# Optimization experiments

Measured on AMD Instinct MI355X. Metric: run time of the kernel, lower is better.

The kernel has to match this reference:

```python
import jax, jax.numpy as jnp
import numpy as np

N_NODES = 100000
N_EDGES = 1200000
D = 64
BN_EPS = 1e-5


def setup_inputs() -> dict:
    key = jax.random.key(0)
    ks = jax.random.split(key, 6)
    x = jax.random.normal(ks[0], (N_NODES, D), dtype=jnp.float32)
    edge_index = jax.random.randint(ks[1], (2, N_EDGES), 0, N_NODES, dtype=jnp.int64)
    # Linear params (Kaiming-uniform style scale)
    lim = 1.0 / np.sqrt(D)
    W = jax.random.uniform(ks[2], (D, D), dtype=jnp.float32, minval=-lim, maxval=lim)
    b = jax.random.uniform(ks[3], (D,), dtype=jnp.float32, minval=-lim, maxval=lim)
    gamma = jnp.ones((D,), dtype=jnp.float32)
    beta = jnp.zeros((D,), dtype=jnp.float32)
    C = jax.random.normal(ks[4], (D, D), dtype=jnp.float32) * 0.1
    return {"x": x, "edge_index": edge_index, "W": W, "b": b,
            "gamma": gamma, "beta": beta, "C": C}


def reference(x, edge_index, W, b, gamma, beta, C):
    n = x.shape[0]
    src, dst = edge_index[0], edge_index[1]
    # SimpleConv(aggr='mean', combine_root='sum'): mean over incoming messages + root
    msg_sum = jax.ops.segment_sum(x[src], dst, num_segments=n)            # [N, D]
    deg = jax.ops.segment_sum(jnp.ones_like(src, dtype=x.dtype), dst, num_segments=n)
    agg = msg_sum / jnp.maximum(deg, 1.0)[:, None]
    h = x + agg
    # Linear
    h = h @ W.T + b
    # BatchNorm1d (training mode: batch stats, biased variance)
    mean = jnp.mean(h, axis=0)
    var = jnp.mean((h - mean) ** 2, axis=0)
    h = (h - mean) * jax.lax.rsqrt(var + BN_EPS) * gamma + beta
    # AsymSwiGLU gate
    gate = jax.nn.sigmoid(h @ C)
    return gate * h
```

## Files before the change

kernel.cpp:

```cpp
#include <hip/hip_runtime.h>
#include <math.h>

#define D 64
#define BN_EPS 1e-5f

#define NBITS 7
#define BINSZ 128
#define MAXBINS 800
#define CAP 2048
#define CHUNK 4096
#define BUCKET 48
#define OP 68
#define WP 72

typedef short bf16x8 __attribute__((ext_vector_type(8)));
typedef float f32x4 __attribute__((ext_vector_type(4)));

__device__ __forceinline__ unsigned f2bf(float f) {
    unsigned u = __float_as_uint(f);
    return (u + 0x7FFFu + ((u >> 16) & 1u)) >> 16;
}
__device__ __forceinline__ float bf2f(unsigned short h) {
    return __uint_as_float(((unsigned)h) << 16);
}
__device__ __forceinline__ bf16x8 cvt8f(const float* __restrict__ p) {
    float4 a = ((const float4*)p)[0];
    float4 b = ((const float4*)p)[1];
    bf16x8 r;
    r[0] = (short)f2bf(a.x); r[1] = (short)f2bf(a.y);
    r[2] = (short)f2bf(a.z); r[3] = (short)f2bf(a.w);
    r[4] = (short)f2bf(b.x); r[5] = (short)f2bf(b.y);
    r[6] = (short)f2bf(b.z); r[7] = (short)f2bf(b.w);
    return r;
}
__device__ __forceinline__ void cvtrow16(const float* __restrict__ src,
                                         unsigned short* dst) {
    float4 a = ((const float4*)src)[0], b = ((const float4*)src)[1];
    float4 c = ((const float4*)src)[2], d = ((const float4*)src)[3];
    uint4 o0, o1;
    o0.x = f2bf(a.x) | (f2bf(a.y) << 16);
    o0.y = f2bf(a.z) | (f2bf(a.w) << 16);
    o0.z = f2bf(b.x) | (f2bf(b.y) << 16);
    o0.w = f2bf(b.z) | (f2bf(b.w) << 16);
    o1.x = f2bf(c.x) | (f2bf(c.y) << 16);
    o1.y = f2bf(c.z) | (f2bf(c.w) << 16);
    o1.z = f2bf(d.x) | (f2bf(d.y) << 16);
    o1.w = f2bf(d.z) | (f2bf(d.w) << 16);
    ((uint4*)dst)[0] = o0;
    ((uint4*)dst)[1] = o1;
}

__global__ __launch_bounds__(256) void xhalf_kernel(
    const float* __restrict__ x, unsigned short* __restrict__ xh, long long n8) {
    long long t = (long long)blockIdx.x * 256 + threadIdx.x;
    if (t >= n8) return;
    const float4* rp = (const float4*)(x + t * 8);
    float4 a = rp[0], b = rp[1];
    uint4 o;
    o.x = f2bf(a.x) | (f2bf(a.y) << 16);
    o.y = f2bf(a.z) | (f2bf(a.w) << 16);
    o.z = f2bf(b.x) | (f2bf(b.y) << 16);
    o.w = f2bf(b.z) | (f2bf(b.w) << 16);
    *(uint4*)(xh + t * 8) = o;
}

__global__ __launch_bounds__(1024) void binA_kernel(
    const int* __restrict__ ei, int* __restrict__ binCursor,
    unsigned* __restrict__ binBuf, int E, int nbins) {
    __shared__ unsigned short pos[CHUNK];
    __shared__ int hist[MAXBINS];
    __shared__ int base[MAXBINS];
    int tid = threadIdx.x;
    int c0 = blockIdx.x * CHUNK;

    for (int i = tid; i < nbins; i += 1024) hist[i] = 0;
    __syncthreads();

#pragma unroll
    for (int k = 0; k < CHUNK / 1024; ++k) {
        int i = k * 1024 + tid;
        int e = c0 + i;
        if (e < E) {
            int dst = ei[E + e];
            pos[i] = (unsigned short)atomicAdd(&hist[dst >> NBITS], 1);
        }
    }
    __syncthreads();

    for (int b = tid; b < nbins; b += 1024) {
        int h = hist[b];
        base[b] = h > 0 ? atomicAdd(&binCursor[b * 16], h) : 0;
    }
    __syncthreads();

#pragma unroll
    for (int k = 0; k < CHUNK / 1024; ++k) {
        int i = k * 1024 + tid;
        int e = c0 + i;
        if (e < E) {
            int src = ei[e];
            int dst = ei[E + e];
            int b = dst >> NBITS;
            int idx = base[b] + (int)pos[i];
            if (idx < CAP)
                binBuf[(size_t)b * CAP + idx] =
                    ((unsigned)src << NBITS) | (unsigned)(dst & (BINSZ - 1));
        }
    }
}

__global__ __launch_bounds__(256) void binSort_kernel(
    const unsigned* __restrict__ binBuf, const int* __restrict__ binCursor,
    int* __restrict__ csr, int* __restrict__ cnt, int N) {
    __shared__ int hist[BINSZ];
    int bin = blockIdx.x, tid = threadIdx.x;
    int nodeBase = bin << NBITS;
    int nrows = N - nodeBase; if (nrows > BINSZ) nrows = BINSZ;
    if (tid < BINSZ) hist[tid] = 0;
    __syncthreads();
    int nE = binCursor[bin * 16]; if (nE > CAP) nE = CAP;
    const unsigned* eb = binBuf + (size_t)bin * CAP;
    for (int i = tid; i < nE; i += 256) {
        unsigned r = eb[i];
        int dl = (int)(r & (BINSZ - 1));
        int src = (int)(r >> NBITS);
        int p = atomicAdd(&hist[dl], 1);
        if (p < BUCKET) csr[(size_t)(nodeBase + dl) * BUCKET + p] = src;
    }
    __syncthreads();
    for (int r = tid; r < nrows; r += 256) cnt[nodeBase + r] = hist[r];
}

__global__ __launch_bounds__(256) void gather_kernel(
    const unsigned short* __restrict__ xh,
    const int* __restrict__ csr, const int* __restrict__ cnt,
    float* __restrict__ hpre, int N) {
    int node = blockIdx.x * 4 + (threadIdx.x >> 6);
    if (node >= N) return;
    int l = threadIdx.x & 63;
    int c = l & 15;
    int g = l >> 4;
    int deg = cnt[node];
    deg = __builtin_amdgcn_readfirstlane(deg);
    int trips = deg < BUCKET ? deg : BUCKET;
    int sidx = l < BUCKET ? csr[(size_t)node * BUCKET + l] : 0;
    float a0 = 0.f, a1 = 0.f, a2 = 0.f, a3 = 0.f;
    if (trips > 0) {
        int nq = (trips + 3) >> 2;
        int last = trips - 1;
        uint2 v[12];
#pragma unroll
        for (int q = 0; q < 12; ++q) {
            if (q < nq) {
                int r = 4 * q + g;
                int rc = r < trips ? r : last;
                int s = __shfl(sidx, rc);
                v[q] = *(const uint2*)(xh + (size_t)s * D + c * 4);
            }
        }
#pragma unroll
        for (int q = 0; q < 12; ++q) {
            if (q < nq) {
                int r = 4 * q + g;
                if (r < trips) {
                    unsigned lo = v[q].x, hi = v[q].y;
                    a0 += __uint_as_float(lo << 16);
                    a1 += __uint_as_float(lo & 0xFFFF0000u);
                    a2 += __uint_as_float(hi << 16);
                    a3 += __uint_as_float(hi & 0xFFFF0000u);
                }
            }
        }
    }
    a0 += __shfl_xor(a0, 16); a0 += __shfl_xor(a0, 32);
    a1 += __shfl_xor(a1, 16); a1 += __shfl_xor(a1, 32);
    a2 += __shfl_xor(a2, 16); a2 += __shfl_xor(a2, 32);
    a3 += __shfl_xor(a3, 16); a3 += __shfl_xor(a3, 32);
    float invd = deg > 0 ? 1.0f / (float)deg : 1.0f;
    if (g == 0) {
        uint2 rt = *(const uint2*)(xh + (size_t)node * D + c * 4);
        float4 o;
        o.x = __uint_as_float(rt.x << 16)         + a0 * invd;
        o.y = __uint_as_float(rt.x & 0xFFFF0000u) + a1 * invd;
        o.z = __uint_as_float(rt.y << 16)         + a2 * invd;
        o.w = __uint_as_float(rt.y & 0xFFFF0000u) + a3 * invd;
        *(float4*)(hpre + (size_t)node * D + c * 4) = o;
    }
}

__global__ __launch_bounds__(256) void linMFMA_kernel(
    float* __restrict__ h, const float* __restrict__ W,
    const float* __restrict__ bias, float* __restrict__ partial, int N) {
    __shared__ float tile[64 * OP];
    __shared__ unsigned short wt[64 * WP];
    __shared__ float psum[4 * 128];
    int tid = threadIdx.x;
    int lane = tid & 63;
    int w = tid >> 6;
    int ar = lane & 15, g = lane >> 4;
    int rbase = blockIdx.x << 6;
    int nrows = N - rbase; if (nrows > 64) nrows = 64;

#pragma unroll
    for (int it = 0; it < 4; ++it) {
        int u = it * 256 + tid;
        int r = u >> 4, c = u & 15;
        float4 v = (r < nrows)
            ? *(const float4*)(h + (size_t)(rbase + r) * D + c * 4)
            : make_float4(0.f, 0.f, 0.f, 0.f);
        *(float4*)(tile + r * OP + c * 4) = v;
    }
    {
        int r = tid >> 2, q = tid & 3;
        cvtrow16(W + (size_t)r * D + q * 16, wt + r * WP + q * 16);
    }
    __syncthreads();

    bool valid = (rbase + w * 16) < N;
    f32x4 acc[4];
    if (valid) {
        const float* arow = tile + (w * 16 + ar) * OP + 8 * g;
        bf16x8 a0 = cvt8f(arow);
        bf16x8 a1 = cvt8f(arow + 32);
#pragma unroll
        for (int t = 0; t < 4; ++t) {
            bf16x8 b0 = *(const bf16x8*)(wt + (t * 16 + ar) * WP + 8 * g);
            bf16x8 b1 = *(const bf16x8*)(wt + (t * 16 + ar) * WP + 32 + 8 * g);
            float bj = bias[t * 16 + ar];
            acc[t][0] = bj; acc[t][1] = bj; acc[t][2] = bj; acc[t][3] = bj;
            acc[t] = __builtin_amdgcn_mfma_f32_16x16x32_bf16(a0, b0, acc[t], 0, 0, 0);
            acc[t] = __builtin_amdgcn_mfma_f32_16x16x32_bf16(a1, b1, acc[t], 0, 0, 0);
        }
    }
    __syncthreads();

    if (valid) {
#pragma unroll
        for (int t = 0; t < 4; ++t) {
#pragma unroll
            for (int r = 0; r < 4; ++r)
                tile[(w * 16 + 4 * g + r) * OP + t * 16 + ar] = acc[t][r];
            float s = acc[t][0] + acc[t][1] + acc[t][2] + acc[t][3];
            float q = acc[t][0] * acc[t][0] + acc[t][1] * acc[t][1] +
                      acc[t][2] * acc[t][2] + acc[t][3] * acc[t][3];
            s += __shfl_xor(s, 16); s += __shfl_xor(s, 32);
            q += __shfl_xor(q, 16); q += __shfl_xor(q, 32);
            if (lane < 16) {
                psum[w * 128 + t * 16 + lane] = s;
                psum[w * 128 + 64 + t * 16 + lane] = q;
            }
        }
    } else {
        psum[w * 128 + lane] = 0.f;
        psum[w * 128 + 64 + lane] = 0.f;
    }
    __syncthreads();

#pragma unroll
    for (int it = 0; it < 4; ++it) {
        int u = it * 256 + tid;
        int r = u >> 4, c = u & 15;
        if (r < nrows)
            *(float4*)(h + (size_t)(rbase + r) * D + c * 4) =
                *(const float4*)(tile + r * OP + c * 4);
    }
    if (tid < 128)
        partial[(size_t)blockIdx.x * 128 + tid] =
            psum[tid] + psum[128 + tid] + psum[256 + tid] + psum[384 + tid];
}

__global__ __launch_bounds__(256) void reduceBN_kernel(
    const float* __restrict__ partial, const float* __restrict__ gamma,
    const float* __restrict__ beta, float* __restrict__ ss,
    int nWG, float inv_n) {
    __shared__ float rs[256], rq[256];
    int f = blockIdx.x;
    int tid = threadIdx.x;
    float s = 0.f, q = 0.f;
    for (int w = tid; w < nWG; w += 256) {
        s += partial[(size_t)w * 128 + f];
        q += partial[(size_t)w * 128 + 64 + f];
    }
    rs[tid] = s; rq[tid] = q;
    __syncthreads();
    for (int st = 128; st > 0; st >>= 1) {
        if (tid < st) { rs[tid] += rs[tid + st]; rq[tid] += rq[tid + st]; }
        __syncthreads();
    }
    if (tid == 0) {
        float mean = rs[0] * inv_n;
        float var = rq[0] * inv_n - mean * mean;
        float rstd = rsqrtf(var + BN_EPS);
        float sc = gamma[f] * rstd;
        ss[f] = sc;
        ss[64 + f] = beta[f] - mean * sc;
    }
}

__global__ __launch_bounds__(256) void gateMFMA_kernel(
    float* __restrict__ h, const float* __restrict__ ss,
    const float* __restrict__ C, int N) {
    __shared__ float tile[64 * OP];
    __shared__ unsigned short ct[64 * WP];
    int tid = threadIdx.x;
    int lane = tid & 63;
    int w = tid >> 6;
    int ar = lane & 15, g = lane >> 4;
    int rbase = blockIdx.x << 6;
    int nrows = N - rbase; if (nrows > 64) nrows = 64;

#pragma unroll
    for (int it = 0; it < 4; ++it) {
        int u = it * 256 + tid;
        int r = u >> 4, c = u & 15;
        float4 v = (r < nrows)
            ? *(const float4*)(h + (size_t)(rbase + r) * D + c * 4)
            : make_float4(0.f, 0.f, 0.f, 0.f);
        *(float4*)(tile + r * OP + c * 4) = v;
    }
    {
        int k = tid >> 2, q = tid & 3;
        const float* cp = C + (size_t)k * D + q * 16;
#pragma unroll
        for (int i = 0; i < 16; ++i)
            ct[(q * 16 + i) * WP + k] = (unsigned short)f2bf(cp[i]);
    }
    __syncthreads();

    bool valid = (rbase + w * 16) < N;
    f32x4 acc[4];
    if (valid) {
        const float* arow = tile + (w * 16 + ar) * OP + 8 * g;
        float4 s0 = *(const float4*)(ss + 8 * g);
        float4 s1 = *(const float4*)(ss + 8 * g + 4);
        float4 o0 = *(const float4*)(ss + 64 + 8 * g);
        float4 o1 = *(const float4*)(ss + 64 + 8 * g + 4);
        float4 v0 = ((const float4*)arow)[0];
        float4 v1 = ((const float4*)arow)[1];
        bf16x8 a0, a1;
        a0[0] = (short)f2bf(v0.x * s0.x + o0.x);
        a0[1] = (short)f2bf(v0.y * s0.y + o0.y);
        a0[2] = (short)f2bf(v0.z * s0.z + o0.z);
        a0[3] = (short)f2bf(v0.w * s0.w + o0.w);
        a0[4] = (short)f2bf(v1.x * s1.x + o1.x);
        a0[5] = (short)f2bf(v1.y * s1.y + o1.y);
        a0[6] = (short)f2bf(v1.z * s1.z + o1.z);
        a0[7] = (short)f2bf(v1.w * s1.w + o1.w);
        float4 t0 = *(const float4*)(ss + 32 + 8 * g);
        float4 t1 = *(const float4*)(ss + 32 + 8 * g + 4);
        float4 u0 = *(const float4*)(ss + 96 + 8 * g);
        float4 u1 = *(const float4*)(ss + 96 + 8 * g + 4);
        float4 w0 = ((const float4*)(arow + 32))[0];
        float4 w1 = ((const float4*)(arow + 32))[1];
        a1[0] = (short)f2bf(w0.x * t0.x + u0.x);
        a1[1] = (short)f2bf(w0.y * t0.y + u0.y);
        a1[2] = (short)f2bf(w0.z * t0.z + u0.z);
        a1[3] = (short)f2bf(w0.w * t0.w + u0.w);
        a1[4] = (short)f2bf(w1.x * t1.x + u1.x);
        a1[5] = (short)f2bf(w1.y * t1.y + u1.y);
        a1[6] = (short)f2bf(w1.z * t1.z + u1.z);
        a1[7] = (short)f2bf(w1.w * t1.w + u1.w);
#pragma unroll
        for (int t = 0; t < 4; ++t) {
            bf16x8 b0 = *(const bf16x8*)(ct + (t * 16 + ar) * WP + 8 * g);
            bf16x8 b1 = *(const bf16x8*)(ct + (t * 16 + ar) * WP + 32 + 8 * g);
            acc[t][0] = 0.f; acc[t][1] = 0.f; acc[t][2] = 0.f; acc[t][3] = 0.f;
            acc[t] = __builtin_amdgcn_mfma_f32_16x16x32_bf16(a0, b0, acc[t], 0, 0, 0);
            acc[t] = __builtin_amdgcn_mfma_f32_16x16x32_bf16(a1, b1, acc[t], 0, 0, 0);
        }
#pragma unroll
        for (int t = 0; t < 4; ++t) {
            float scC = ss[t * 16 + ar];
            float shC = ss[64 + t * 16 + ar];
#pragma unroll
            for (int r = 0; r < 4; ++r) {
                int idx = (w * 16 + 4 * g + r) * OP + t * 16 + ar;
                float hn = tile[idx] * scC + shC;
                float gg = 1.0f / (1.0f + __expf(-acc[t][r]));
                tile[idx] = gg * hn;
            }
        }
    }
    __syncthreads();

#pragma unroll
    for (int it = 0; it < 4; ++it) {
        int u = it * 256 + tid;
        int r = u >> 4, c = u & 15;
        if (r < nrows)
            *(float4*)(h + (size_t)(rbase + r) * D + c * 4) =
                *(const float4*)(tile + r * OP + c * 4);
    }
}

extern "C" void kernel_launch(void* const* d_in, const int* in_sizes, int n_in,
                              void* d_out, int out_size, void* d_ws, size_t ws_size,
                              hipStream_t stream) {
    const float* x     = (const float*)d_in[0];
    const int*   ei    = (const int*)d_in[1];
    const float* W     = (const float*)d_in[2];
    const float* b     = (const float*)d_in[3];
    const float* gamma = (const float*)d_in[4];
    const float* beta  = (const float*)d_in[5];
    const float* C     = (const float*)d_in[6];
    float* out = (float*)d_out;

    const int N = in_sizes[0] / D;
    const int E = in_sizes[1] / 2;
    const int nbins = (N + BINSZ - 1) >> NBITS;
    const int nWGlin = (N + 63) / 64;

    int*            binCursor = (int*)d_ws;
    float*          ss        = (float*)(binCursor + (size_t)nbins * 16);
    int*            cnt       = (int*)(ss + 128);
    int*            csr       = cnt + N;
    unsigned*       binBuf    = (unsigned*)(csr + (size_t)N * BUCKET);
    float*          partial   = (float*)(binBuf + (size_t)nbins * CAP);
    unsigned short* xh        = (unsigned short*)(partial + (size_t)nWGlin * 128);

    hipMemsetAsync(d_ws, 0, ((size_t)nbins * 16 + 128) * sizeof(int), stream);

    {
        long long n8 = (long long)N * D / 8;
        xhalf_kernel<<<(int)((n8 + 255) / 256), 256, 0, stream>>>(x, xh, n8);
    }
    binA_kernel<<<(E + CHUNK - 1) / CHUNK, 1024, 0, stream>>>(ei, binCursor, binBuf, E, nbins);
    binSort_kernel<<<nbins, 256, 0, stream>>>(binBuf, binCursor, csr, cnt, N);
    gather_kernel<<<(N + 3) / 4, 256, 0, stream>>>(xh, csr, cnt, out, N);
    linMFMA_kernel<<<nWGlin, 256, 0, stream>>>(out, W, b, partial, N);
    reduceBN_kernel<<<64, 256, 0, stream>>>(partial, gamma, beta, ss, nWGlin, 1.0f / (float)N);
    gateMFMA_kernel<<<(N + 63) / 64, 256, 0, stream>>>(out, ss, C, N);
}
```

Baseline: 116.9 us.

## Fuse neighbor gather with linear MFMA and BN partial sums

Merges the gather kernel and the linear MFMA kernel into a single 1024-thread kernel. Each block gathers 64 node rows straight into shared memory, then 16 waves each compute one 16x16 output tile with MFMA. The fp32 pre-linear activations no longer make a round trip through global memory, and one launch is removed. In exchange, the large blocks may limit occupancy and lose some latency hiding for the irregular gathers, and each wave now processes 4 nodes serially.

```diff
diff --git a/kernel.cpp b/kernel.cpp
--- a/kernel.cpp
+++ b/kernel.cpp
@@ -32,22 +32,6 @@
     r[4] = (short)f2bf(b.x); r[5] = (short)f2bf(b.y);
     r[6] = (short)f2bf(b.z); r[7] = (short)f2bf(b.w);
     return r;
-}
-__device__ __forceinline__ void cvtrow16(const float* __restrict__ src,
-                                         unsigned short* dst) {
-    float4 a = ((const float4*)src)[0], b = ((const float4*)src)[1];
-    float4 c = ((const float4*)src)[2], d = ((const float4*)src)[3];
-    uint4 o0, o1;
-    o0.x = f2bf(a.x) | (f2bf(a.y) << 16);
-    o0.y = f2bf(a.z) | (f2bf(a.w) << 16);
-    o0.z = f2bf(b.x) | (f2bf(b.y) << 16);
-    o0.w = f2bf(b.z) | (f2bf(b.w) << 16);
-    o1.x = f2bf(c.x) | (f2bf(c.y) << 16);
-    o1.y = f2bf(c.z) | (f2bf(c.w) << 16);
-    o1.z = f2bf(d.x) | (f2bf(d.y) << 16);
-    o1.w = f2bf(d.z) | (f2bf(d.w) << 16);
-    ((uint4*)dst)[0] = o0;
-    ((uint4*)dst)[1] = o1;
 }
 
 __global__ __launch_bounds__(256) void xhalf_kernel(
@@ -131,142 +115,135 @@
     for (int r = tid; r < nrows; r += 256) cnt[nodeBase + r] = hist[r];
 }
 
-__global__ __launch_bounds__(256) void gather_kernel(
-    const unsigned short* __restrict__ xh,
-    const int* __restrict__ csr, const int* __restrict__ cnt,
-    float* __restrict__ hpre, int N) {
-    int node = blockIdx.x * 4 + (threadIdx.x >> 6);
-    if (node >= N) return;
-    int l = threadIdx.x & 63;
-    int c = l & 15;
-    int g = l >> 4;
-    int deg = cnt[node];
-    deg = __builtin_amdgcn_readfirstlane(deg);
-    int trips = deg < BUCKET ? deg : BUCKET;
-    int sidx = l < BUCKET ? csr[(size_t)node * BUCKET + l] : 0;
-    float a0 = 0.f, a1 = 0.f, a2 = 0.f, a3 = 0.f;
-    if (trips > 0) {
-        int nq = (trips + 3) >> 2;
-        int last = trips - 1;
-        uint2 v[12];
-#pragma unroll
-        for (int q = 0; q < 12; ++q) {
-            if (q < nq) {
-                int r = 4 * q + g;
-                int rc = r < trips ? r : last;
-                int s = __shfl(sidx, rc);
-                v[q] = *(const uint2*)(xh + (size_t)s * D + c * 4);
-            }
-        }
-#pragma unroll
-        for (int q = 0; q < 12; ++q) {
-            if (q < nq) {
-                int r = 4 * q + g;
-                if (r < trips) {
-                    unsigned lo = v[q].x, hi = v[q].y;
-                    a0 += __uint_as_float(lo << 16);
-                    a1 += __uint_as_float(lo & 0xFFFF0000u);
-                    a2 += __uint_as_float(hi << 16);
-                    a3 += __uint_as_float(hi & 0xFFFF0000u);
-                }
-            }
-        }
-    }
-    a0 += __shfl_xor(a0, 16); a0 += __shfl_xor(a0, 32);
-    a1 += __shfl_xor(a1, 16); a1 += __shfl_xor(a1, 32);
-    a2 += __shfl_xor(a2, 16); a2 += __shfl_xor(a2, 32);
-    a3 += __shfl_xor(a3, 16); a3 += __shfl_xor(a3, 32);
-    float invd = deg > 0 ? 1.0f / (float)deg : 1.0f;
-    if (g == 0) {
-        uint2 rt = *(const uint2*)(xh + (size_t)node * D + c * 4);
-        float4 o;
-        o.x = __uint_as_float(rt.x << 16)         + a0 * invd;
-        o.y = __uint_as_float(rt.x & 0xFFFF0000u) + a1 * invd;
-        o.z = __uint_as_float(rt.y << 16)         + a2 * invd;
-        o.w = __uint_as_float(rt.y & 0xFFFF0000u) + a3 * invd;
-        *(float4*)(hpre + (size_t)node * D + c * 4) = o;
-    }
-}
-
-__global__ __launch_bounds__(256) void linMFMA_kernel(
-    float* __restrict__ h, const float* __restrict__ W,
-    const float* __restrict__ bias, float* __restrict__ partial, int N) {
+__global__ __launch_bounds__(1024) void fusedGL_kernel(
+    const unsigned short* __restrict__ xh, const int* __restrict__ csr,
+    const int* __restrict__ cnt, const float* __restrict__ W,
+    const float* __restrict__ bias, float* __restrict__ h,
+    float* __restrict__ partial, int N) {
     __shared__ float tile[64 * OP];
     __shared__ unsigned short wt[64 * WP];
-    __shared__ float psum[4 * 128];
+    __shared__ float psum[16 * 32];
     int tid = threadIdx.x;
     int lane = tid & 63;
     int w = tid >> 6;
-    int ar = lane & 15, g = lane >> 4;
     int rbase = blockIdx.x << 6;
     int nrows = N - rbase; if (nrows > 64) nrows = 64;
 
-#pragma unroll
-    for (int it = 0; it < 4; ++it) {
-        int u = it * 256 + tid;
-        int r = u >> 4, c = u & 15;
-        float4 v = (r < nrows)
-            ? *(const float4*)(h + (size_t)(rbase + r) * D + c * 4)
-            : make_float4(0.f, 0.f, 0.f, 0.f);
-        *(float4*)(tile + r * OP + c * 4) = v;
-    }
     {
-        int r = tid >> 2, q = tid & 3;
-        cvtrow16(W + (size_t)r * D + q * 16, wt + r * WP + q * 16);
-    }
-    __syncthreads();
-
-    bool valid = (rbase + w * 16) < N;
-    f32x4 acc[4];
-    if (valid) {
-        const float* arow = tile + (w * 16 + ar) * OP + 8 * g;
-        bf16x8 a0 = cvt8f(arow);
-        bf16x8 a1 = cvt8f(arow + 32);
-#pragma unroll
-        for (int t = 0; t < 4; ++t) {
-            bf16x8 b0 = *(const bf16x8*)(wt + (t * 16 + ar) * WP + 8 * g);
-            bf16x8 b1 = *(const bf16x8*)(wt + (t * 16 + ar) * WP + 32 + 8 * g);
-            float bj = bias[t * 16 + ar];
-            acc[t][0] = bj; acc[t][1] = bj; acc[t][2] = bj; acc[t][3] = bj;
-            acc[t] = __builtin_amdgcn_mfma_f32_16x16x32_bf16(a0, b0, acc[t], 0, 0, 0);
-            acc[t] = __builtin_amdgcn_mfma_f32_16x16x32_bf16(a1, b1, acc[t], 0, 0, 0);
+        int r = tid >> 4, q = tid & 15;
+        float4 v = *(const float4*)(W + (size_t)r * D + q * 4);
+        uint2 o;
+        o.x = f2bf(v.x) | (f2bf(v.y) << 16);
+        o.y = f2bf(v.z) | (f2bf(v.w) << 16);
+        *(uint2*)(wt + r * WP + q * 4) = o;
+    }
+
+    int c = lane & 15, g = lane >> 4;
+    for (int i = 0; i < 4; ++i) {
+        int nl = w * 4 + i;
+        int node = rbase + nl;
+        if (node < N) {
+            int deg = cnt[node];
+            deg = __builtin_amdgcn_readfirstlane(deg);
+            int trips = deg < BUCKET ? deg : BUCKET;
+            int sidx = lane < BUCKET ? csr[(size_t)node * BUCKET + lane] : 0;
+            float a0 = 0.f, a1 = 0.f, a2 = 0.f, a3 = 0.f;
+            if (trips > 0) {
+                int nq = (trips + 3) >> 2;
+                int last = trips - 1;
+                uint2 v[12];
+#pragma unroll
+                for (int q = 0; q < 12; ++q) {
+                    if (q < nq) {
+                        int r = 4 * q + g;
+                        int rc = r < trips ? r : last;
+                        int s = __shfl(sidx, rc);
+                        v[q] = *(const uint2*)(xh + (size_t)s * D + c * 4);
+                    }
+                }
+#pragma unroll
+                for (int q = 0; q < 12; ++q) {
+                    if (q < nq) {
+                        int r = 4 * q + g;
+                        if (r < trips) {
+                            unsigned lo = v[q].x, hi = v[q].y;
+                            a0 += __uint_as_float(lo << 16);
+                            a1 += __uint_as_float(lo & 0xFFFF0000u);
+                            a2 += __uint_as_float(hi << 16);
+                            a3 += __uint_as_float(hi & 0xFFFF0000u);
+                        }
+                    }
+                }
+            }
+            a0 += __shfl_xor(a0, 16); a0 += __shfl_xor(a0, 32);
+            a1 += __shfl_xor(a1, 16); a1 += __shfl_xor(a1, 32);
+            a2 += __shfl_xor(a2, 16); a2 += __shfl_xor(a2, 32);
+            a3 += __shfl_xor(a3, 16); a3 += __shfl_xor(a3, 32);
+            float invd = deg > 0 ? 1.0f / (float)deg : 1.0f;
+            if (g == 0) {
+                uint2 rt = *(const uint2*)(xh + (size_t)node * D + c * 4);
+                float4 o;
+                o.x = __uint_as_float(rt.x << 16)         + a0 * invd;
+                o.y = __uint_as_float(rt.x & 0xFFFF0000u) + a1 * invd;
+                o.z = __uint_as_float(rt.y << 16)         + a2 * invd;
+                o.w = __uint_as_float(rt.y & 0xFFFF0000u) + a3 * invd;
+                *(float4*)(tile + nl * OP + c * 4) = o;
+            }
+        } else {
+            if (g == 0)
+                *(float4*)(tile + nl * OP + c * 4) = make_float4(0.f, 0.f, 0.f, 0.f);
         }
     }
     __syncthreads();
 
-    if (valid) {
-#pragma unroll
-        for (int t = 0; t < 4; ++t) {
-#pragma unroll
-            for (int r = 0; r < 4; ++r)
-                tile[(w * 16 + 4 * g + r) * OP + t * 16 + ar] = acc[t][r];
-            float s = acc[t][0] + acc[t][1] + acc[t][2] + acc[t][3];
-            float q = acc[t][0] * acc[t][0] + acc[t][1] * acc[t][1] +
-                      acc[t][2] * acc[t][2] + acc[t][3] * acc[t][3];
-            s += __shfl_xor(s, 16); s += __shfl_xor(s, 32);
-            q += __shfl_xor(q, 16); q += __shfl_xor(q, 32);
-            if (lane < 16) {
-                psum[w * 128 + t * 16 + lane] = s;
-                psum[w * 128 + 64 + t * 16 + lane] = q;
-            }
-        }
-    } else {
-        psum[w * 128 + lane] = 0.f;
-        psum[w * 128 + 64 + lane] = 0.f;
-    }
-    __syncthreads();
-
-#pragma unroll
-    for (int it = 0; it < 4; ++it) {
-        int u = it * 256 + tid;
-        int r = u >> 4, c = u & 15;
+    int rb = w & 3, t = w >> 2;
+    int ar = lane & 15, gg = lane >> 4;
+    const float* arow = tile + (rb * 16 + ar) * OP + 8 * gg;
+    bf16x8 A0 = cvt8f(arow);
+    bf16x8 A1 = cvt8f(arow + 32);
+    bf16x8 B0 = *(const bf16x8*)(wt + (t * 16 + ar) * WP + 8 * gg);
+    bf16x8 B1 = *(const bf16x8*)(wt + (t * 16 + ar) * WP + 32 + 8 * gg);
+    float bj = bias[t * 16 + ar];
+    f32x4 acc;
+    acc[0] = bj; acc[1] = bj; acc[2] = bj; acc[3] = bj;
+    acc = __builtin_amdgcn_mfma_f32_16x16x32_bf16(A0, B0, acc, 0, 0, 0);
+    acc = __builtin_amdgcn_mfma_f32_16x16x32_bf16(A1, B1, acc, 0, 0, 0);
+    __syncthreads();
+
+#pragma unroll
+    for (int r = 0; r < 4; ++r)
+        tile[(rb * 16 + 4 * gg + r) * OP + t * 16 + ar] = acc[r];
+    float s = 0.f, q = 0.f;
+#pragma unroll
+    for (int r = 0; r < 4; ++r) {
+        int row = rb * 16 + 4 * gg + r;
+        float v = (row < nrows) ? acc[r] : 0.f;
+        s += v; q += v * v;
+    }
+    s += __shfl_xor(s, 16); s += __shfl_xor(s, 32);
+    q += __shfl_xor(q, 16); q += __shfl_xor(q, 32);
+    if (lane < 16) {
+        psum[w * 32 + lane] = s;
+        psum[w * 32 + 16 + lane] = q;
+    }
+    __syncthreads();
+
+    {
+        int r = tid >> 4, cq = tid & 15;
         if (r < nrows)
-            *(float4*)(h + (size_t)(rbase + r) * D + c * 4) =
-                *(const float4*)(tile + r * OP + c * 4);
-    }
-    if (tid < 128)
-        partial[(size_t)blockIdx.x * 128 + tid] =
-            psum[tid] + psum[128 + tid] + psum[256 + tid] + psum[384 + tid];
+            *(float4*)(h + (size_t)(rbase + r) * D + cq * 4) =
+                *(const float4*)(tile + r * OP + cq * 4);
+    }
+    if (tid < 128) {
+        int f = tid & 63;
+        int off = (tid >= 64) ? 16 : 0;
+        int t2 = f >> 4, col = f & 15;
+        float a = 0.f;
+#pragma unroll
+        for (int rb2 = 0; rb2 < 4; ++rb2)
+            a += psum[(t2 * 4 + rb2) * 32 + off + col];
+        partial[(size_t)blockIdx.x * 128 + tid] = a;
+    }
 }
 
 __global__ __launch_bounds__(256) void reduceBN_kernel(
@@ -426,8 +403,7 @@
     }
     binA_kernel<<<(E + CHUNK - 1) / CHUNK, 1024, 0, stream>>>(ei, binCursor, binBuf, E, nbins);
     binSort_kernel<<<nbins, 256, 0, stream>>>(binBuf, binCursor, csr, cnt, N);
-    gather_kernel<<<(N + 3) / 4, 256, 0, stream>>>(xh, csr, cnt, out, N);
-    linMFMA_kernel<<<nWGlin, 256, 0, stream>>>(out, W, b, partial, N);
+    fusedGL_kernel<<<nWGlin, 1024, 0, stream>>>(xh, csr, cnt, W, b, out, partial, N);
     reduceBN_kernel<<<64, 256, 0, stream>>>(partial, gamma, beta, ss, nWGlin, 1.0f / (float)N);
     gateMFMA_kernel<<<(N + 63) / 64, 256, 0, stream>>>(out, ss, C, N);
 }
```

Measured after the change: 117.6 us. No clear change (+0.6%).
